# Kernel tuning notes

Hardware: AMD Instinct MI355X
Metric: run time of the kernel (lower is better)

## Reference

```python
import jax, jax.numpy as jnp
import numpy as np
import math

N_USERS, N_ENTITIES, DIMS, N_REL = 50000, 100000, 64, 16
E_KG, E_IN = 1_500_000, 1_000_000
N_HEADS = 2
D_K = DIMS // N_HEADS


def setup_inputs() -> dict:
    key = jax.random.key(0)
    ks = jax.random.split(key, 9)
    user_emb = 0.1 * jax.random.normal(ks[0], (N_USERS, DIMS), jnp.float32)
    entity_emb = 0.1 * jax.random.normal(ks[1], (N_ENTITIES, DIMS), jnp.float32)
    edge_index = jax.random.randint(ks[2], (2, E_KG), 0, N_ENTITIES)
    edge_type = jax.random.randint(ks[3], (E_KG,), 1, N_REL + 1)  # 1-indexed as in original
    inter_user = jax.random.randint(ks[4], (E_IN,), 0, N_USERS)
    inter_item = jax.random.randint(ks[5], (E_IN,), 0, N_ENTITIES)
    inter_edge = jnp.stack([inter_user, inter_item], axis=0)
    inter_edge_w = jax.random.uniform(ks[6], (E_IN,), jnp.float32)
    relation_emb = 0.1 * jax.random.normal(ks[7], (N_REL, DIMS), jnp.float32)
    W_Q = 0.1 * jax.random.normal(ks[8], (DIMS, DIMS), jnp.float32)
    return {
        'layers_num': 2,
        'user_emb': user_emb,
        'entity_emb': entity_emb,
        'inter_edge': inter_edge,
        'inter_edge_w': inter_edge_w,
        'edge_index': edge_index,
        'edge_type': edge_type,
        'relation_emb': relation_emb,
        'W_Q': W_Q,
    }


def _agg_layer(user_emb, entity_emb, edge_index, edge_type, inter_edge, inter_edge_w,
               relation_emb, W_Q):
    n_ent = entity_emb.shape[0]
    n_usr = user_emb.shape[0]
    head, tail = edge_index[0], edge_index[1]
    rel = relation_emb[edge_type - 1]                        # [E, D]
    head_emb = entity_emb[head]                              # [E, D]
    tail_emb = entity_emb[tail]                              # [E, D]
    q = (head_emb @ W_Q).reshape(-1, N_HEADS, D_K)           # [E, H, d_k]
    k = (tail_emb @ W_Q).reshape(-1, N_HEADS, D_K) * rel.reshape(-1, N_HEADS, D_K)
    score = jnp.sum(q * k, axis=-1) * (1.0 / math.sqrt(D_K)) # [E, H]
    # scatter_softmax over segments defined by head
    seg_max = jax.ops.segment_max(score, head, num_segments=n_ent)   # [N, H]
    ex = jnp.exp(score - seg_max[head])
    seg_sum = jax.ops.segment_sum(ex, head, num_segments=n_ent)
    attn = ex / seg_sum[head]                                # [E, H]
    value = (tail_emb * rel).reshape(-1, N_HEADS, D_K)       # [E, H, d_k]
    msg = (value * attn[..., None]).reshape(-1, DIMS)        # [E, D]
    entity_agg = jax.ops.segment_sum(msg, head, num_segments=n_ent)  # [N, D]
    # F.normalize: L2 along dim 1 with eps=1e-12
    norm = jnp.linalg.norm(entity_agg, axis=1, keepdims=True)
    entity_agg = entity_agg / jnp.maximum(norm, 1e-12)
    # user <- item aggregation
    item_agg = inter_edge_w[:, None] * entity_emb[inter_edge[1]]
    user_agg = jax.ops.segment_sum(item_agg, inter_edge[0], num_segments=n_usr)
    # entity <- user aggregation
    u2i = inter_edge_w[:, None] * user_emb[inter_edge[0]]
    entity_agg = entity_agg + jax.ops.segment_sum(u2i, inter_edge[1], num_segments=n_ent)
    return entity_agg, user_agg


def reference(layers_num, user_emb, entity_emb, inter_edge, inter_edge_w,
              edge_index, edge_type, relation_emb, W_Q):
    user_embs = [user_emb]
    entity_embs = [entity_emb]
    for _ in range(layers_num):
        entity_emb, user_emb = _agg_layer(user_emb, entity_emb, edge_index, edge_type,
                                          inter_edge, inter_edge_w, relation_emb, W_Q)
        user_embs.append(user_emb)
        entity_embs.append(entity_emb)
    user_out = jnp.mean(jnp.stack(user_embs, axis=1), axis=1)
    entity_out = jnp.mean(jnp.stack(entity_embs, axis=1), axis=1)
    return (user_out, entity_out)
```

## Files before the change

kernel.cpp:

```cpp
#include <hip/hip_runtime.h>
#include <hip/hip_fp16.h>

#define NU 50000
#define NE 100000
#define DIM 64
#define NRELS 16
#define EKG 1500000
#define EIN 1000000

#define KG_CHUNK 8192
#define KG_NBUCK ((NE + 511) >> 9)
#define B8_CHUNK 4096
#define KG_CAP 9216
#define C8_CAP 6656

#define NEB (NE / 4)
#define NUB (NU / 4)

#define NB_BKG ((EKG + KG_CHUNK - 1) / KG_CHUNK)
#define NB_B8  ((EIN + B8_CHUNK - 1) / B8_CHUNK)
#define NB_CKG KG_NBUCK
#define NB_CUI ((NU + 255) >> 8)
#define NB_CIU ((NE + 511) >> 9)

typedef _Float16 f16x2 __attribute__((ext_vector_type(2)));

union U16 { int4 v; __half2 h[4]; };
union H4 { int2 i2; __half2 h[2]; };

__device__ __forceinline__ float fdot2a(__half2 a, __half2 b, float c) {
#if __has_builtin(__builtin_amdgcn_fdot2)
    union { __half2 h; f16x2 v; } ua, ub;
    ua.h = a; ub.h = b;
    return __builtin_amdgcn_fdot2(ua.v, ub.v, c, false);
#else
    return c + __half2float(a.x) * __half2float(b.x) + __half2float(a.y) * __half2float(b.y);
#endif
}

__device__ __forceinline__ float dpp_red4(float p) {
    int t;
    t = __builtin_amdgcn_update_dpp(0, __float_as_int(p), 0xB1, 0xF, 0xF, true);
    p += __int_as_float(t);
    t = __builtin_amdgcn_update_dpp(0, __float_as_int(p), 0x4E, 0xF, 0xF, true);
    p += __int_as_float(t);
    return p;
}

__global__ void k_castH(const float4* __restrict__ u4, const float4* __restrict__ r4,
                        int2* __restrict__ uH, int2* __restrict__ rH) {
    int i = blockIdx.x * blockDim.x + threadIdx.x;
    if (i < NU * 16) {
        float4 v = u4[i];
        H4 o; o.h[0] = __floats2half2_rn(v.x, v.y); o.h[1] = __floats2half2_rn(v.z, v.w);
        uH[i] = o.i2;
    }
    if (i < NRELS * 16) {
        float4 v = r4[i];
        H4 o; o.h[0] = __floats2half2_rn(v.x, v.y); o.h[1] = __floats2half2_rn(v.z, v.w);
        rH[i] = o.i2;
    }
}

__global__ __launch_bounds__(256) void k_gemm_f(const float* __restrict__ ent,
                                                const float* __restrict__ wq,
                                                __half* __restrict__ qmH,
                                                __half* __restrict__ entH) {
    __shared__ float sW[64 * 64];
    __shared__ float sR[16 * 64];
    int t = threadIdx.x;
    for (int i = t; i < 4096; i += 256) sW[i] = wq[i];
    long row0 = (long)blockIdx.x * 16;
    for (int i = t; i < 1024; i += 256) sR[i] = ent[row0 * 64 + i];
    __syncthreads();
    int r = t >> 4, cg = t & 15;
    const float4* sW4 = (const float4*)sW;
    const float4* sR4 = (const float4*)sR;
    float4 acc = {0.f, 0.f, 0.f, 0.f};
#pragma unroll
    for (int k = 0; k < 64; k++) {
        float a = sR[r * 64 + k];
        float4 wv = sW4[k * 16 + cg];
        acc.x += a * wv.x; acc.y += a * wv.y; acc.z += a * wv.z; acc.w += a * wv.w;
    }
    H4 o;
    o.h[0] = __floats2half2_rn(acc.x, acc.y);
    o.h[1] = __floats2half2_rn(acc.z, acc.w);
    ((int2*)qmH)[(row0 + r) * 16 + cg] = o.i2;
    float4 ev = sR4[r * 16 + cg];
    H4 e;
    e.h[0] = __floats2half2_rn(ev.x, ev.y);
    e.h[1] = __floats2half2_rn(ev.z, ev.w);
    ((int2*)entH)[(row0 + r) * 16 + cg] = e.i2;
}

__global__ __launch_bounds__(256) void k_gemm_h(const __half* __restrict__ ent,
                                                const float* __restrict__ wq,
                                                __half* __restrict__ qmH) {
    __shared__ float sW[64 * 64];
    __shared__ float sR[16 * 64];
    int t = threadIdx.x;
    for (int i = t; i < 4096; i += 256) sW[i] = wq[i];
    long row0 = (long)blockIdx.x * 16;
    const __half2* e2 = (const __half2*)ent;
    for (int i = t; i < 512; i += 256) {
        float2 f = __half22float2(e2[row0 * 32 + i]);
        sR[2 * i] = f.x; sR[2 * i + 1] = f.y;
    }
    __syncthreads();
    int r = t >> 4, cg = t & 15;
    const float4* sW4 = (const float4*)sW;
    float4 acc = {0.f, 0.f, 0.f, 0.f};
#pragma unroll
    for (int k = 0; k < 64; k++) {
        float a = sR[r * 64 + k];
        float4 wv = sW4[k * 16 + cg];
        acc.x += a * wv.x; acc.y += a * wv.y; acc.z += a * wv.z; acc.w += a * wv.w;
    }
    H4 o;
    o.h[0] = __floats2half2_rn(acc.x, acc.y);
    o.h[1] = __floats2half2_rn(acc.z, acc.w);
    ((int2*)qmH)[(row0 + r) * 16 + cg] = o.i2;
}

__global__ __launch_bounds__(256) void k_hist_bucket(const int* __restrict__ eh,
        const int* __restrict__ iu, const int* __restrict__ ii,
        int* __restrict__ cntK, int* __restrict__ cntU, int* __restrict__ cntI) {
    __shared__ int sK[256], sU[256], sI[256];
    int t = threadIdx.x;
    sK[t] = 0; sU[t] = 0; sI[t] = 0;
    __syncthreads();
    int stride = gridDim.x * 256;
    for (int e = blockIdx.x * 256 + t; e < EKG; e += stride)
        atomicAdd(&sK[eh[e] >> 9], 1);
    for (int e = blockIdx.x * 256 + t; e < EIN; e += stride) {
        atomicAdd(&sU[iu[e] >> 8], 1);
        atomicAdd(&sI[ii[e] >> 9], 1);
    }
    __syncthreads();
    if (sK[t]) atomicAdd(&cntK[t], sK[t]);
    if (sU[t]) atomicAdd(&cntU[t], sU[t]);
    if (sI[t]) atomicAdd(&cntI[t], sI[t]);
}

__global__ __launch_bounds__(256) void k_bucket_scan(const int* __restrict__ cntK,
        const int* __restrict__ cntU, const int* __restrict__ cntI,
        int* __restrict__ kg_boff, int* __restrict__ ui_boff, int* __restrict__ iu_boff,
        int* __restrict__ kg_g, int* __restrict__ ui_g, int* __restrict__ iu_g) {
    __shared__ int sc[256];
    int t = threadIdx.x;
#define SCAN1(cnt, boff, gcur) { \
    int v = cnt[t]; sc[t] = v; __syncthreads(); \
    for (int o = 1; o < 256; o <<= 1) { \
        int u = (t >= o) ? sc[t - o] : 0; __syncthreads(); sc[t] += u; __syncthreads(); } \
    int e = sc[t] - v; boff[t] = e; gcur[t] = e; \
    __syncthreads(); }
    SCAN1(cntK, kg_boff, kg_g)
    SCAN1(cntU, ui_boff, ui_g)
    SCAN1(cntI, iu_boff, iu_g)
#undef SCAN1
}

struct SmB {
    union {
        struct { unsigned stage[KG_CHUNK]; int dest[KG_CHUNK]; } kg;
        struct { int2 stage[B8_CHUNK]; int dest[B8_CHUNK]; } b8;
    } u;
};

__device__ __forceinline__ void binB8_body(const int* __restrict__ key,
        const int* __restrict__ aux, const float* __restrict__ wv, int nE,
        int shift, int auxShift, int* __restrict__ gcur, int2* __restrict__ tmp,
        int cb, int2* stage, int* dest,
        int* cnt, int* boff, int* gbase, int* curl, int* sc) {
    int t = threadIdx.x;
    int base = cb * B8_CHUNK;
    int nloc = nE - base; if (nloc > B8_CHUNK) nloc = B8_CHUNK;
    cnt[t] = 0;
    __syncthreads();
    for (int i = t; i < nloc; i += 256)
        atomicAdd(&cnt[key[base + i] >> shift], 1);
    __syncthreads();
    int v = cnt[t];
    sc[t] = v;
    __syncthreads();
    for (int o = 1; o < 256; o <<= 1) {
        int u = (t >= o) ? sc[t - o] : 0;
        __syncthreads();
        sc[t] += u;
        __syncthreads();
    }
    boff[t] = sc[t] - v;
    curl[t] = sc[t] - v;
    gbase[t] = atomicAdd(&gcur[t], v);
    __syncthreads();
    int lowmask = (1 << shift) - 1;
    for (int i = t; i < nloc; i += 256) {
        int e = base + i;
        int k = key[e];
        int b = k >> shift;
        int2 pay;
        pay.x = aux[e] | ((k & lowmask) << auxShift);
        pay.y = __float_as_int(wv[e]);
        int pos = atomicAdd(&curl[b], 1);
        stage[pos] = pay;
        dest[pos] = gbase[b] + (pos - boff[b]);
    }
    __syncthreads();
    for (int s = t; s < nloc; s += 256) tmp[dest[s]] = stage[s];
}

__global__ __launch_bounds__(256) void k_binB_all(const int* __restrict__ eh,
        const int* __restrict__ et, const int* __restrict__ ety,
        int* __restrict__ kg_g, unsigned* __restrict__ kg_tmp,
        const int* __restrict__ iu, const int* __restrict__ ii,
        const float* __restrict__ iwf,
        int* __restrict__ ui_g, int2* __restrict__ ui_tmp,
        int* __restrict__ iu_g, int2* __restrict__ iu_tmp) {
    __shared__ SmB sm;
    __shared__ int cnt[256], boff[256], gbase[256], curl[256], sc[256];
    int bid = blockIdx.x;
    int t = threadIdx.x;
    if (bid < NB_BKG) {
        int base = bid * KG_CHUNK;
        int nloc = EKG - base; if (nloc > KG_CHUNK) nloc = KG_CHUNK;
        for (int i = t; i < KG_NBUCK; i += 256) cnt[i] = 0;
        __syncthreads();
        for (int i = t; i < nloc; i += 256)
            atomicAdd(&cnt[eh[base + i] >> 9], 1);
        __syncthreads();
        int v = (t < KG_NBUCK) ? cnt[t] : 0;
        sc[t] = v;
        __syncthreads();
        for (int o = 1; o < 256; o <<= 1) {
            int u = (t >= o) ? sc[t - o] : 0;
            __syncthreads();
            sc[t] += u;
            __syncthreads();
        }
        if (t < KG_NBUCK) {
            boff[t] = sc[t] - v;
            curl[t] = sc[t] - v;
            gbase[t] = atomicAdd(&kg_g[t], v);
        }
        __syncthreads();
        for (int i = t; i < nloc; i += 256) {
            int e = base + i;
            int h = eh[e];
            int b = h >> 9;
            unsigned pay = (unsigned)et[e] | ((unsigned)(ety[e] - 1) << 17)
                         | ((unsigned)(h & 511) << 21);
            int pos = atomicAdd(&curl[b], 1);
            sm.u.kg.stage[pos] = pay;
            sm.u.kg.dest[pos] = gbase[b] + (pos - boff[b]);
        }
        __syncthreads();
        for (int s = t; s < nloc; s += 256) kg_tmp[sm.u.kg.dest[s]] = sm.u.kg.stage[s];
    } else if (bid < NB_BKG + NB_B8) {
        binB8_body(iu, ii, iwf, EIN, 8, 17, ui_g, ui_tmp, bid - NB_BKG,
                   sm.u.b8.stage, sm.u.b8.dest, cnt, boff, gbase, curl, sc);
    } else {
        binB8_body(ii, iu, iwf, EIN, 9, 16, iu_g, iu_tmp, bid - NB_BKG - NB_B8,
                   sm.u.b8.stage, sm.u.b8.dest, cnt, boff, gbase, curl, sc);
    }
}

struct SmC {
    union {
        unsigned kgstage[KG_CAP];
        int2 c8stage[C8_CAP];
    } u;
};

__device__ __forceinline__ void binC8_body(const int2* __restrict__ tmp,
        const int* __restrict__ boffg, int2* __restrict__ dst, int* __restrict__ off,
        int nnodes, int shift, int auxShift, int lb, int nb,
        int2* stage, int* curl, int* sc) {
    int b = lb;
    int nbase = b << shift;
    int nlim = nnodes - nbase; if (nlim > (1 << shift)) nlim = 1 << shift;
    if (nlim <= 0) return;
    int t = threadIdx.x;
    int r0 = boffg[b];
    int r1 = boffg[b + 1];
    int cntb = r1 - r0;
    int lowmask = (1 << shift) - 1;
    curl[t] = 0; curl[t + 256] = 0;
    __syncthreads();
    for (int s = t; s < cntb; s += 256)
        atomicAdd(&curl[(tmp[r0 + s].x >> auxShift) & lowmask], 1);
    __syncthreads();
    int v0 = curl[2 * t], v1 = curl[2 * t + 1];
    int s2 = v0 + v1;
    sc[t] = s2;
    __syncthreads();
    for (int o = 1; o < 256; o <<= 1) {
        int u = (t >= o) ? sc[t - o] : 0;
        __syncthreads();
        sc[t] += u;
        __syncthreads();
    }
    int excl = sc[t] - s2;
    curl[2 * t] = excl;
    curl[2 * t + 1] = excl + v0;
    if (2 * t < nlim) off[nbase + 2 * t] = r0 + excl;
    if (2 * t + 1 < nlim) off[nbase + 2 * t + 1] = r0 + excl + v0;
    if (b == nb - 1 && t == 0) off[nbase + nlim] = r1;
    __syncthreads();
    if (cntb <= C8_CAP) {
        for (int s = t; s < cntb; s += 256) {
            int2 pay = tmp[r0 + s];
            int l = (pay.x >> auxShift) & lowmask;
            int pos = atomicAdd(&curl[l], 1);
            stage[pos] = pay;
        }
        __syncthreads();
        for (int s = t; s < cntb; s += 256) dst[r0 + s] = stage[s];
    } else {
        for (int s = t; s < cntb; s += 256) {
            int2 pay = tmp[r0 + s];
            int l = (pay.x >> auxShift) & lowmask;
            int pos = atomicAdd(&curl[l], 1);
            dst[r0 + pos] = pay;
        }
    }
}

__global__ __launch_bounds__(256) void k_binC_all(const unsigned* __restrict__ kg_tmp,
        const int* __restrict__ kg_boff, unsigned* __restrict__ kg_tr, int* __restrict__ kg_off,
        const int2* __restrict__ ui_tmp, const int* __restrict__ ui_boff,
        int2* __restrict__ ui_iw, int* __restrict__ ui_off,
        const int2* __restrict__ iu_tmp, const int* __restrict__ iu_boff,
        int2* __restrict__ iu_iw, int* __restrict__ iu_off) {
    __shared__ SmC sm;
    __shared__ int curl[512];
    __shared__ int sc[256];
    int bid = blockIdx.x;
    int t = threadIdx.x;
    if (bid < NB_CKG) {
        int b = bid;
        int nbase = b << 9;
        int nlim = NE - nbase; if (nlim > 512) nlim = 512;
        if (nlim <= 0) return;
        int r0 = kg_boff[b];
        int r1 = kg_boff[b + 1];
        int cntb = r1 - r0;
        curl[t] = 0; curl[t + 256] = 0;
        __syncthreads();
        for (int s = t; s < cntb; s += 256)
            atomicAdd(&curl[(kg_tmp[r0 + s] >> 21) & 511], 1);
        __syncthreads();
        int v0 = curl[2 * t], v1 = curl[2 * t + 1];
        int s2 = v0 + v1;
        sc[t] = s2;
        __syncthreads();
        for (int o = 1; o < 256; o <<= 1) {
            int u = (t >= o) ? sc[t - o] : 0;
            __syncthreads();
            sc[t] += u;
            __syncthreads();
        }
        int excl = sc[t] - s2;
        curl[2 * t] = excl;
        curl[2 * t + 1] = excl + v0;
        if (2 * t < nlim) kg_off[nbase + 2 * t] = r0 + excl;
        if (2 * t + 1 < nlim) kg_off[nbase + 2 * t + 1] = r0 + excl + v0;
        if (b == NB_CKG - 1 && t == 0) kg_off[nbase + nlim] = r1;
        __syncthreads();
        if (cntb <= KG_CAP) {
            for (int s = t; s < cntb; s += 256) {
                unsigned pay = kg_tmp[r0 + s];
                int l = (pay >> 21) & 511;
                int pos = atomicAdd(&curl[l], 1);
                sm.u.kgstage[pos] = pay;
            }
            __syncthreads();
            for (int s = t; s < cntb; s += 256) kg_tr[r0 + s] = sm.u.kgstage[s];
        } else {
            for (int s = t; s < cntb; s += 256) {
                unsigned pay = kg_tmp[r0 + s];
                int l = (pay >> 21) & 511;
                int pos = atomicAdd(&curl[l], 1);
                kg_tr[r0 + pos] = pay;
            }
        }
    } else if (bid < NB_CKG + NB_CUI) {
        binC8_body(ui_tmp, ui_boff, ui_iw, ui_off, NU, 8, 17,
                   bid - NB_CKG, NB_CUI, sm.u.c8stage, curl, sc);
    } else {
        binC8_body(iu_tmp, iu_boff, iu_iw, iu_off, NE, 9, 16,
                   bid - NB_CKG - NB_CUI, NB_CIU, sm.u.c8stage, curl, sc);
    }
}

template<bool FIRST, bool FINAL>
__global__ __launch_bounds__(256) void k_layer(const __half* __restrict__ qmH,
        const __half* __restrict__ relH, const __half* __restrict__ entH,
        const __half* __restrict__ usrH,
        const int* __restrict__ kg_off, const unsigned* __restrict__ kg_tr,
        const int* __restrict__ iu_off, const int2* __restrict__ iu_iw,
        const int* __restrict__ ui_off, const int2* __restrict__ ui_iw,
        float* __restrict__ eacc, __half* __restrict__ entHout,
        float* __restrict__ uacc, __half* __restrict__ usrHout,
        const float* __restrict__ ent0, const float* __restrict__ usr0,
        float* __restrict__ out) {
    int w = __builtin_amdgcn_readfirstlane(threadIdx.x >> 6);
    int lane = threadIdx.x & 63;
    int sub = lane >> 3;
    int li  = lane & 7;
    const float SC = 0.17677669529663687f;
    const float NEG = -1e30f;
    const float inv3 = 1.f / 3.f;
    const int4* qmI  = (const int4*)qmH;
    const int4* entI = (const int4*)entH;
    const int4* relI = (const int4*)relH;
    const int4* usrI = (const int4*)usrH;

    if (blockIdx.x < NEB) {
        int node = blockIdx.x * 4 + w;
        U16 qh; qh.v = qmI[(long)node * 8 + li];
        int b0 = kg_off[node], b1 = kg_off[node + 1];
        int deg = b1 - b0;

        float ssum = 0.f;
        float acc[8] = {0.f, 0.f, 0.f, 0.f, 0.f, 0.f, 0.f, 0.f};
        if (deg > 0) {
            int s = b0;
            int i0 = s + sub;
            unsigned tr = kg_tr[i0 < b1 ? i0 : b1 - 1];
            for (; s < b1; s += 8) {
                int ni = s + 8 + sub;
                unsigned trn = kg_tr[ni < b1 ? ni : b1 - 1];
                bool has = (s + sub) < b1;
                int tl = tr & 0x1FFFF, rr = (tr >> 17) & 15;
                U16 rl; rl.v = relI[rr * 8 + li];
                U16 qt; qt.v = qmI[(long)tl * 8 + li];
                U16 ev; ev.v = entI[(long)tl * 8 + li];
                float p = 0.f;
#pragma unroll
                for (int k = 0; k < 4; k++) {
                    __half2 kk = __hmul2(qt.h[k], rl.h[k]);
                    p = fdot2a(qh.h[k], kk, p);
                }
                p = dpp_red4(p);
                float e = __expf(has ? p * SC : NEG);
                ssum += e;
#pragma unroll
                for (int k = 0; k < 4; k++) {
                    __half2 v2 = __hmul2(ev.h[k], rl.h[k]);
                    float2 vf = __half22float2(v2);
                    acc[2 * k]     += vf.x * e;
                    acc[2 * k + 1] += vf.y * e;
                }
                tr = trn;
            }
#pragma unroll
            for (int o = 8; o <= 32; o <<= 1) {
                ssum += __shfl_xor(ssum, o, 64);
#pragma unroll
                for (int k = 0; k < 8; k++) acc[k] += __shfl_xor(acc[k], o, 64);
            }
            float inv = 1.f / ssum;
#pragma unroll
            for (int k = 0; k < 8; k++) acc[k] *= inv;
            float ss = 0.f;
#pragma unroll
            for (int k = 0; k < 8; k++) ss += acc[k] * acc[k];
            ss += __shfl_xor(ss, 1, 64);
            ss += __shfl_xor(ss, 2, 64);
            ss += __shfl_xor(ss, 4, 64);
            float nsc = 1.f / fmaxf(sqrtf(ss), 1e-12f);
#pragma unroll
            for (int k = 0; k < 8; k++) acc[k] *= nsc;
        }

        int c0 = iu_off[node], c1 = iu_off[node + 1];
        if (c1 > c0) {
            float ua[8] = {0.f, 0.f, 0.f, 0.f, 0.f, 0.f, 0.f, 0.f};
            int t2 = c0;
            int j0 = t2 + sub;
            int2 pw = iu_iw[j0 < c1 ? j0 : c1 - 1];
            for (; t2 < c1; t2 += 8) {
                int nj = t2 + 8 + sub;
                int2 pwn = iu_iw[nj < c1 ? nj : c1 - 1];
                bool has = (t2 + sub) < c1;
                float wv = has ? __int_as_float(pw.y) : 0.f;
                U16 uu; uu.v = usrI[(long)(pw.x & 0xFFFF) * 8 + li];
#pragma unroll
                for (int k = 0; k < 4; k++) {
                    float2 uf = __half22float2(uu.h[k]);
                    ua[2 * k]     += wv * uf.x;
                    ua[2 * k + 1] += wv * uf.y;
                }
                pw = pwn;
            }
#pragma unroll
            for (int o = 8; o <= 32; o <<= 1) {
#pragma unroll
                for (int k = 0; k < 8; k++) ua[k] += __shfl_xor(ua[k], o, 64);
            }
#pragma unroll
            for (int k = 0; k < 8; k++) acc[k] += ua[k];
        }

        if (sub == 0) {
            long base = (long)node * 16 + 2 * li;
            float4* eacc4 = (float4*)eacc;
            float4 e0, e1;
            if (FIRST) {
                e0.x = acc[0]; e0.y = acc[1]; e0.z = acc[2]; e0.w = acc[3];
                e1.x = acc[4]; e1.y = acc[5]; e1.z = acc[6]; e1.w = acc[7];
            } else {
                e0 = eacc4[base]; e1 = eacc4[base + 1];
                e0.x += acc[0]; e0.y += acc[1]; e0.z += acc[2]; e0.w += acc[3];
                e1.x += acc[4]; e1.y += acc[5]; e1.z += acc[6]; e1.w += acc[7];
            }
            if (!FINAL) {
                eacc4[base] = e0; eacc4[base + 1] = e1;
                U16 ho;
                ho.h[0] = __floats2half2_rn(acc[0], acc[1]);
                ho.h[1] = __floats2half2_rn(acc[2], acc[3]);
                ho.h[2] = __floats2half2_rn(acc[4], acc[5]);
                ho.h[3] = __floats2half2_rn(acc[6], acc[7]);
                ((int4*)entHout)[(long)node * 8 + li] = ho.v;
            } else {
                const float4* a4 = (const float4*)ent0;
                float4 a0 = a4[base], a1 = a4[base + 1];
                float4 o0, o1;
                o0.x = (a0.x + e0.x) * inv3; o0.y = (a0.y + e0.y) * inv3;
                o0.z = (a0.z + e0.z) * inv3; o0.w = (a0.w + e0.w) * inv3;
                o1.x = (a1.x + e1.x) * inv3; o1.y = (a1.y + e1.y) * inv3;
                o1.z = (a1.z + e1.z) * inv3; o1.w = (a1.w + e1.w) * inv3;
                float4* oute = (float4*)out + (long)NU * 16;
                oute[base] = o0; oute[base + 1] = o1;
            }
        }
    } else {
        int node = (blockIdx.x - NEB) * 4 + w;
        int b0 = ui_off[node], b1 = ui_off[node + 1];
        float ax[8] = {0.f, 0.f, 0.f, 0.f, 0.f, 0.f, 0.f, 0.f};
        if (b1 > b0) {
            int s = b0;
            int j0 = s + sub;
            int2 pw = ui_iw[j0 < b1 ? j0 : b1 - 1];
            for (; s < b1; s += 8) {
                int nj = s + 8 + sub;
                int2 pwn = ui_iw[nj < b1 ? nj : b1 - 1];
                bool has = (s + sub) < b1;
                float wv = has ? __int_as_float(pw.y) : 0.f;
                U16 uu; uu.v = entI[(long)(pw.x & 0x1FFFF) * 8 + li];
#pragma unroll
                for (int k = 0; k < 4; k++) {
                    float2 uf = __half22float2(uu.h[k]);
                    ax[2 * k]     += wv * uf.x;
                    ax[2 * k + 1] += wv * uf.y;
                }
                pw = pwn;
            }
#pragma unroll
            for (int o = 8; o <= 32; o <<= 1) {
#pragma unroll
                for (int k = 0; k < 8; k++) ax[k] += __shfl_xor(ax[k], o, 64);
            }
        }
        if (sub == 0) {
            long base = (long)node * 16 + 2 * li;
            float4* uacc4 = (float4*)uacc;
            float4 u0, u1;
            if (FIRST) {
                u0.x = ax[0]; u0.y = ax[1]; u0.z = ax[2]; u0.w = ax[3];
                u1.x = ax[4]; u1.y = ax[5]; u1.z = ax[6]; u1.w = ax[7];
            } else {
                u0 = uacc4[base]; u1 = uacc4[base + 1];
                u0.x += ax[0]; u0.y += ax[1]; u0.z += ax[2]; u0.w += ax[3];
                u1.x += ax[4]; u1.y += ax[5]; u1.z += ax[6]; u1.w += ax[7];
            }
            if (!FINAL) {
                uacc4[base] = u0; uacc4[base + 1] = u1;
                U16 ho;
                ho.h[0] = __floats2half2_rn(ax[0], ax[1]);
                ho.h[1] = __floats2half2_rn(ax[2], ax[3]);
                ho.h[2] = __floats2half2_rn(ax[4], ax[5]);
                ho.h[3] = __floats2half2_rn(ax[6], ax[7]);
                ((int4*)usrHout)[(long)node * 8 + li] = ho.v;
            } else {
                const float4* a4 = (const float4*)usr0;
                float4 a0 = a4[base], a1 = a4[base + 1];
                float4 o0, o1;
                o0.x = (a0.x + u0.x) * inv3; o0.y = (a0.y + u0.y) * inv3;
                o0.z = (a0.z + u0.z) * inv3; o0.w = (a0.w + u0.w) * inv3;
                o1.x = (a1.x + u1.x) * inv3; o1.y = (a1.y + u1.y) * inv3;
                o1.z = (a1.z + u1.z) * inv3; o1.w = (a1.w + u1.w) * inv3;
                float4* outu = (float4*)out;
                outu[base] = o0; outu[base + 1] = o1;
            }
        }
    }
}

extern "C" void kernel_launch(void* const* d_in, const int* in_sizes, int n_in,
                              void* d_out, int out_size, void* d_ws, size_t ws_size,
                              hipStream_t stream) {
    const float* usr0  = (const float*)d_in[1];
    const float* ent0  = (const float*)d_in[2];
    const int*   inter = (const int*)d_in[3];
    const float* iwf   = (const float*)d_in[4];
    const int*   eidx  = (const int*)d_in[5];
    const int*   etype = (const int*)d_in[6];
    const float* relf  = (const float*)d_in[7];
    const float* wqf   = (const float*)d_in[8];
    float* out = (float*)d_out;

    const int* eh = eidx;
    const int* et = eidx + EKG;
    const int* iu = inter;
    const int* ii = inter + EIN;

    float* p = (float*)d_ws;
    float* eacc = p;  p += (long)NE * DIM;
    float* uacc = p;  p += (long)NU * DIM;
    __half* qmH   = (__half*)p;  p += (long)NE * DIM / 2;
    __half* entHa = (__half*)p;  p += (long)NE * DIM / 2;
    __half* entHb = (__half*)p;  p += (long)NE * DIM / 2;
    __half* usrHa = (__half*)p;  p += (long)NU * DIM / 2;
    __half* usrHb = (__half*)p;  p += (long)NU * DIM / 2;
    __half* relH  = (__half*)p;  p += (long)NRELS * DIM / 2;
    int* cntK = (int*)p;        p += 256;
    int* cntU = (int*)p;        p += 256;
    int* cntI = (int*)p;        p += 256;
    int* kg_boff = (int*)p;     p += 256;
    int* ui_boff = (int*)p;     p += 256;
    int* iu_boff = (int*)p;     p += 256;
    int* kg_off = (int*)p;      p += NE + 2;
    int* ui_off = (int*)p;      p += NU + 2;
    int* iu_off = (int*)p;      p += NE + 2;
    int* kg_g   = (int*)p;      p += 256;
    int* ui_g   = (int*)p;      p += 256;
    int* iu_g   = (int*)p;      p += 256;
    unsigned* kg_tr  = (unsigned*)p; p += EKG;
    unsigned* kg_tmp = (unsigned*)p; p += EKG;
    int2* ui_iw  = (int2*)p;    p += (long)EIN * 2;
    int2* ui_tmp = (int2*)p;    p += (long)EIN * 2;
    int2* iu_iw  = (int2*)p;    p += (long)EIN * 2;
    int2* iu_tmp = (int2*)p;    p += (long)EIN * 2;

    const int B = 256;

    hipMemsetAsync(cntK, 0, (size_t)768 * 4, stream);
    k_castH<<<(NU * 16 + B - 1) / B, B, 0, stream>>>((const float4*)usr0, (const float4*)relf,
                                                     (int2*)usrHa, (int2*)relH);

    k_hist_bucket<<<512, 256, 0, stream>>>(eh, iu, ii, cntK, cntU, cntI);
    k_bucket_scan<<<1, 256, 0, stream>>>(cntK, cntU, cntI, kg_boff, ui_boff, iu_boff,
                                         kg_g, ui_g, iu_g);
    k_binB_all<<<NB_BKG + NB_B8 + NB_B8, 256, 0, stream>>>(eh, et, etype, kg_g, kg_tmp,
                                                           iu, ii, iwf,
                                                           ui_g, ui_tmp, iu_g, iu_tmp);
    k_binC_all<<<NB_CKG + NB_CUI + NB_CIU, 256, 0, stream>>>(kg_tmp, kg_boff, kg_tr, kg_off,
                                                             ui_tmp, ui_boff, ui_iw, ui_off,
                                                             iu_tmp, iu_boff, iu_iw, iu_off);

    k_gemm_f<<<NE / 16, 256, 0, stream>>>(ent0, wqf, qmH, entHa);
    k_layer<true, false><<<NEB + NUB, 256, 0, stream>>>(qmH, relH, entHa, usrHa,
                                                        kg_off, kg_tr, iu_off, iu_iw,
                                                        ui_off, ui_iw,
                                                        eacc, entHb, uacc, usrHb,
                                                        nullptr, nullptr, nullptr);
    k_gemm_h<<<NE / 16, 256, 0, stream>>>(entHb, wqf, qmH);
    k_layer<false, true><<<NEB + NUB, 256, 0, stream>>>(qmH, relH, entHb, usrHb,
                                                        kg_off, kg_tr, iu_off, iu_iw,
                                                        ui_off, ui_iw,
                                                        eacc, nullptr, uacc, nullptr,
                                                        ent0, usr0, out);
}
```

Before: 474.3 us.

## Merge prep kernels into one launch and accumulate aggregations in packed half2

Fuses the histogram, fp16 cast and first-layer GEMM kernels into one block-indexed prep kernel, removing two launches and letting the independent work run side by side. Separately, the per-edge accumulations in the layer kernel (KG attention values, item-user and user-item sums) now use packed half2 FMA instead of fp32 accumulation. This cuts the ALU instruction count in the gather loops but accumulates in fp16, which risks precision loss on high-degree nodes.

Result: no change. 467.2 us (-1.5%).

```diff
diff --git a/kernel.cpp b/kernel.cpp
--- a/kernel.cpp
+++ b/kernel.cpp
@@ -22,6 +22,10 @@
 #define NB_CKG KG_NBUCK
 #define NB_CUI ((NU + 255) >> 8)
 #define NB_CIU ((NE + 511) >> 9)
+
+#define NB_PREP_H 512
+#define NB_PREP_C 3125
+#define NB_PREP_G (NE / 16)
 
 typedef _Float16 f16x2 __attribute__((ext_vector_type(2)));
 
@@ -47,51 +51,74 @@
     return p;
 }
 
-__global__ void k_castH(const float4* __restrict__ u4, const float4* __restrict__ r4,
-                        int2* __restrict__ uH, int2* __restrict__ rH) {
-    int i = blockIdx.x * blockDim.x + threadIdx.x;
-    if (i < NU * 16) {
-        float4 v = u4[i];
-        H4 o; o.h[0] = __floats2half2_rn(v.x, v.y); o.h[1] = __floats2half2_rn(v.z, v.w);
-        uH[i] = o.i2;
-    }
-    if (i < NRELS * 16) {
-        float4 v = r4[i];
-        H4 o; o.h[0] = __floats2half2_rn(v.x, v.y); o.h[1] = __floats2half2_rn(v.z, v.w);
-        rH[i] = o.i2;
-    }
-}
-
-__global__ __launch_bounds__(256) void k_gemm_f(const float* __restrict__ ent,
-                                                const float* __restrict__ wq,
-                                                __half* __restrict__ qmH,
-                                                __half* __restrict__ entH) {
-    __shared__ float sW[64 * 64];
-    __shared__ float sR[16 * 64];
+struct SmP {
+    union {
+        struct { int sK[256], sU[256], sI[256]; } h;
+        struct { float sW[64 * 64]; float sR[16 * 64]; } g;
+    } u;
+};
+
+__global__ __launch_bounds__(256) void k_prep(const int* __restrict__ eh,
+        const int* __restrict__ iu, const int* __restrict__ ii,
+        int* __restrict__ cntK, int* __restrict__ cntU, int* __restrict__ cntI,
+        const float4* __restrict__ u4, const float4* __restrict__ r4,
+        int2* __restrict__ uH, int2* __restrict__ rH,
+        const float* __restrict__ ent, const float* __restrict__ wq,
+        __half* __restrict__ qmH, __half* __restrict__ entH) {
+    __shared__ SmP sm;
+    int bid = blockIdx.x;
     int t = threadIdx.x;
-    for (int i = t; i < 4096; i += 256) sW[i] = wq[i];
-    long row0 = (long)blockIdx.x * 16;
-    for (int i = t; i < 1024; i += 256) sR[i] = ent[row0 * 64 + i];
-    __syncthreads();
-    int r = t >> 4, cg = t & 15;
-    const float4* sW4 = (const float4*)sW;
-    const float4* sR4 = (const float4*)sR;
-    float4 acc = {0.f, 0.f, 0.f, 0.f};
-#pragma unroll
-    for (int k = 0; k < 64; k++) {
-        float a = sR[r * 64 + k];
-        float4 wv = sW4[k * 16 + cg];
-        acc.x += a * wv.x; acc.y += a * wv.y; acc.z += a * wv.z; acc.w += a * wv.w;
-    }
-    H4 o;
-    o.h[0] = __floats2half2_rn(acc.x, acc.y);
-    o.h[1] = __floats2half2_rn(acc.z, acc.w);
-    ((int2*)qmH)[(row0 + r) * 16 + cg] = o.i2;
-    float4 ev = sR4[r * 16 + cg];
-    H4 e;
-    e.h[0] = __floats2half2_rn(ev.x, ev.y);
-    e.h[1] = __floats2half2_rn(ev.z, ev.w);
-    ((int2*)entH)[(row0 + r) * 16 + cg] = e.i2;
+    if (bid < NB_PREP_H) {
+        sm.u.h.sK[t] = 0; sm.u.h.sU[t] = 0; sm.u.h.sI[t] = 0;
+        __syncthreads();
+        int stride = NB_PREP_H * 256;
+        for (int e = bid * 256 + t; e < EKG; e += stride)
+            atomicAdd(&sm.u.h.sK[eh[e] >> 9], 1);
+        for (int e = bid * 256 + t; e < EIN; e += stride) {
+            atomicAdd(&sm.u.h.sU[iu[e] >> 8], 1);
+            atomicAdd(&sm.u.h.sI[ii[e] >> 9], 1);
+        }
+        __syncthreads();
+        if (sm.u.h.sK[t]) atomicAdd(&cntK[t], sm.u.h.sK[t]);
+        if (sm.u.h.sU[t]) atomicAdd(&cntU[t], sm.u.h.sU[t]);
+        if (sm.u.h.sI[t]) atomicAdd(&cntI[t], sm.u.h.sI[t]);
+    } else if (bid < NB_PREP_H + NB_PREP_C) {
+        int i = (bid - NB_PREP_H) * 256 + t;
+        if (i < NU * 16) {
+            float4 v = u4[i];
+            H4 o; o.h[0] = __floats2half2_rn(v.x, v.y); o.h[1] = __floats2half2_rn(v.z, v.w);
+            uH[i] = o.i2;
+        }
+        if (i < NRELS * 16) {
+            float4 v = r4[i];
+            H4 o; o.h[0] = __floats2half2_rn(v.x, v.y); o.h[1] = __floats2half2_rn(v.z, v.w);
+            rH[i] = o.i2;
+        }
+    } else {
+        for (int i = t; i < 4096; i += 256) sm.u.g.sW[i] = wq[i];
+        long row0 = (long)(bid - NB_PREP_H - NB_PREP_C) * 16;
+        for (int i = t; i < 1024; i += 256) sm.u.g.sR[i] = ent[row0 * 64 + i];
+        __syncthreads();
+        int r = t >> 4, cg = t & 15;
+        const float4* sW4 = (const float4*)sm.u.g.sW;
+        const float4* sR4 = (const float4*)sm.u.g.sR;
+        float4 acc = {0.f, 0.f, 0.f, 0.f};
+#pragma unroll
+        for (int k = 0; k < 64; k++) {
+            float a = sm.u.g.sR[r * 64 + k];
+            float4 wv = sW4[k * 16 + cg];
+            acc.x += a * wv.x; acc.y += a * wv.y; acc.z += a * wv.z; acc.w += a * wv.w;
+        }
+        H4 o;
+        o.h[0] = __floats2half2_rn(acc.x, acc.y);
+        o.h[1] = __floats2half2_rn(acc.z, acc.w);
+        ((int2*)qmH)[(row0 + r) * 16 + cg] = o.i2;
+        float4 ev = sR4[r * 16 + cg];
+        H4 e;
+        e.h[0] = __floats2half2_rn(ev.x, ev.y);
+        e.h[1] = __floats2half2_rn(ev.z, ev.w);
+        ((int2*)entH)[(row0 + r) * 16 + cg] = e.i2;
+    }
 }
 
 __global__ __launch_bounds__(256) void k_gemm_h(const __half* __restrict__ ent,
@@ -121,26 +148,6 @@
     o.h[0] = __floats2half2_rn(acc.x, acc.y);
     o.h[1] = __floats2half2_rn(acc.z, acc.w);
     ((int2*)qmH)[(row0 + r) * 16 + cg] = o.i2;
-}
-
-__global__ __launch_bounds__(256) void k_hist_bucket(const int* __restrict__ eh,
-        const int* __restrict__ iu, const int* __restrict__ ii,
-        int* __restrict__ cntK, int* __restrict__ cntU, int* __restrict__ cntI) {
-    __shared__ int sK[256], sU[256], sI[256];
-    int t = threadIdx.x;
-    sK[t] = 0; sU[t] = 0; sI[t] = 0;
-    __syncthreads();
-    int stride = gridDim.x * 256;
-    for (int e = blockIdx.x * 256 + t; e < EKG; e += stride)
-        atomicAdd(&sK[eh[e] >> 9], 1);
-    for (int e = blockIdx.x * 256 + t; e < EIN; e += stride) {
-        atomicAdd(&sU[iu[e] >> 8], 1);
-        atomicAdd(&sI[ii[e] >> 9], 1);
-    }
-    __syncthreads();
-    if (sK[t]) atomicAdd(&cntK[t], sK[t]);
-    if (sU[t]) atomicAdd(&cntU[t], sU[t]);
-    if (sI[t]) atomicAdd(&cntI[t], sI[t]);
 }
 
 __global__ __launch_bounds__(256) void k_bucket_scan(const int* __restrict__ cntK,
@@ -415,6 +422,7 @@
     const int4* entI = (const int4*)entH;
     const int4* relI = (const int4*)relH;
     const int4* usrI = (const int4*)usrH;
+    const __half2 hz = __floats2half2_rn(0.f, 0.f);
 
     if (blockIdx.x < NEB) {
         int node = blockIdx.x * 4 + w;
@@ -425,6 +433,7 @@
         float ssum = 0.f;
         float acc[8] = {0.f, 0.f, 0.f, 0.f, 0.f, 0.f, 0.f, 0.f};
         if (deg > 0) {
+            __half2 acc_h[4] = {hz, hz, hz, hz};
             int s = b0;
             int i0 = s + sub;
             unsigned tr = kg_tr[i0 < b1 ? i0 : b1 - 1];
@@ -445,14 +454,16 @@
                 p = dpp_red4(p);
                 float e = __expf(has ? p * SC : NEG);
                 ssum += e;
-#pragma unroll
-                for (int k = 0; k < 4; k++) {
-                    __half2 v2 = __hmul2(ev.h[k], rl.h[k]);
-                    float2 vf = __half22float2(v2);
-                    acc[2 * k]     += vf.x * e;
-                    acc[2 * k + 1] += vf.y * e;
-                }
+                __half2 e2 = __float2half2_rn(e);
+#pragma unroll
+                for (int k = 0; k < 4; k++)
+                    acc_h[k] = __hfma2(__hmul2(ev.h[k], rl.h[k]), e2, acc_h[k]);
                 tr = trn;
+            }
+#pragma unroll
+            for (int k = 0; k < 4; k++) {
+                float2 vf = __half22float2(acc_h[k]);
+                acc[2 * k] = vf.x; acc[2 * k + 1] = vf.y;
             }
 #pragma unroll
             for (int o = 8; o <= 32; o <<= 1) {
@@ -476,7 +487,7 @@
 
         int c0 = iu_off[node], c1 = iu_off[node + 1];
         if (c1 > c0) {
-            float ua[8] = {0.f, 0.f, 0.f, 0.f, 0.f, 0.f, 0.f, 0.f};
+            __half2 ua_h[4] = {hz, hz, hz, hz};
             int t2 = c0;
             int j0 = t2 + sub;
             int2 pw = iu_iw[j0 < c1 ? j0 : c1 - 1];
@@ -485,14 +496,18 @@
                 int2 pwn = iu_iw[nj < c1 ? nj : c1 - 1];
                 bool has = (t2 + sub) < c1;
                 float wv = has ? __int_as_float(pw.y) : 0.f;
+                __half2 wv2 = __float2half2_rn(wv);
                 U16 uu; uu.v = usrI[(long)(pw.x & 0xFFFF) * 8 + li];
 #pragma unroll
-                for (int k = 0; k < 4; k++) {
-                    float2 uf = __half22float2(uu.h[k]);
-                    ua[2 * k]     += wv * uf.x;
-                    ua[2 * k + 1] += wv * uf.y;
-                }
+                for (int k = 0; k < 4; k++)
+                    ua_h[k] = __hfma2(uu.h[k], wv2, ua_h[k]);
                 pw = pwn;
+            }
+            float ua[8];
+#pragma unroll
+            for (int k = 0; k < 4; k++) {
+                float2 uf = __half22float2(ua_h[k]);
+                ua[2 * k] = uf.x; ua[2 * k + 1] = uf.y;
             }
 #pragma unroll
             for (int o = 8; o <= 32; o <<= 1) {
@@ -540,6 +555,7 @@
         int b0 = ui_off[node], b1 = ui_off[node + 1];
         float ax[8] = {0.f, 0.f, 0.f, 0.f, 0.f, 0.f, 0.f, 0.f};
         if (b1 > b0) {
+            __half2 ax_h[4] = {hz, hz, hz, hz};
             int s = b0;
             int j0 = s + sub;
             int2 pw = ui_iw[j0 < b1 ? j0 : b1 - 1];
@@ -548,14 +564,17 @@
                 int2 pwn = ui_iw[nj < b1 ? nj : b1 - 1];
                 bool has = (s + sub) < b1;
                 float wv = has ? __int_as_float(pw.y) : 0.f;
+                __half2 wv2 = __float2half2_rn(wv);
                 U16 uu; uu.v = entI[(long)(pw.x & 0x1FFFF) * 8 + li];
 #pragma unroll
-                for (int k = 0; k < 4; k++) {
-                    float2 uf = __half22float2(uu.h[k]);
-                    ax[2 * k]     += wv * uf.x;
-                    ax[2 * k + 1] += wv * uf.y;
-                }
+                for (int k = 0; k < 4; k++)
+                    ax_h[k] = __hfma2(uu.h[k], wv2, ax_h[k]);
                 pw = pwn;
+            }
+#pragma unroll
+            for (int k = 0; k < 4; k++) {
+                float2 uf = __half22float2(ax_h[k]);
+                ax[2 * k] = uf.x; ax[2 * k + 1] = uf.y;
             }
 #pragma unroll
             for (int o = 8; o <= 32; o <<= 1) {
@@ -644,13 +663,13 @@
     int2* iu_iw  = (int2*)p;    p += (long)EIN * 2;
     int2* iu_tmp = (int2*)p;    p += (long)EIN * 2;
 
-    const int B = 256;
-
     hipMemsetAsync(cntK, 0, (size_t)768 * 4, stream);
-    k_castH<<<(NU * 16 + B - 1) / B, B, 0, stream>>>((const float4*)usr0, (const float4*)relf,
-                                                     (int2*)usrHa, (int2*)relH);
-
-    k_hist_bucket<<<512, 256, 0, stream>>>(eh, iu, ii, cntK, cntU, cntI);
+
+    k_prep<<<NB_PREP_H + NB_PREP_C + NB_PREP_G, 256, 0, stream>>>(
+        eh, iu, ii, cntK, cntU, cntI,
+        (const float4*)usr0, (const float4*)relf, (int2*)usrHa, (int2*)relH,
+        ent0, wqf, qmH, entHa);
+
     k_bucket_scan<<<1, 256, 0, stream>>>(cntK, cntU, cntI, kg_boff, ui_boff, iu_boff,
                                          kg_g, ui_g, iu_g);
     k_binB_all<<<NB_BKG + NB_B8 + NB_B8, 256, 0, stream>>>(eh, et, etype, kg_g, kg_tmp,
@@ -660,7 +679,6 @@
                                                              ui_tmp, ui_boff, ui_iw, ui_off,
                                                              iu_tmp, iu_boff, iu_iw, iu_off);
 
-    k_gemm_f<<<NE / 16, 256, 0, stream>>>(ent0, wqf, qmH, entHa);
     k_layer<true, false><<<NEB + NUB, 256, 0, stream>>>(qmH, relH, entHa, usrHa,
                                                         kg_off, kg_tr, iu_off, iu_iw,
                                                         ui_off, ui_iw,
```
